# Performance work log

Hardware: AMD Instinct MI355X
Metric: run time of the kernel (lower is better)

## Reference

```python
import jax, jax.numpy as jnp
import numpy as np

BINS = 256
EPS = 1e-8


def _norm255(x):
    # (x - min) / (max - min) * 255, truncated to int (torch .int())
    mx = jnp.max(x, axis=(2, 3), keepdims=True)
    mn = jnp.min(x, axis=(2, 3), keepdims=True)
    return ((x - mn) / (mx - mn) * 255.0).astype(jnp.int32)


def _hist256(x):
    # x int32 [B,C,H,W] -> per-(b,c) 256-bin histogram [B,C,256] float32
    B, C = x.shape[0], x.shape[1]
    flat = x.reshape(B * C, -1)
    rows = jnp.arange(B * C)[:, None]
    h = jnp.zeros((B * C, BINS), jnp.float32).at[rows, flat].add(1.0)
    return h.reshape(B, C, BINS)


def _entropy(x):
    # faithful to Entropy(): p = hist / (H*W); h = -sum p*log(p+1e-8)
    B, C, H, W = x.shape
    p = _hist256(x) / (H * W)
    h = -jnp.sum(p * jnp.log(p + EPS), axis=2)
    return h[:, :, None, None]  # [B,C,1,1]


def _joint_entropy(x_p, x_ms):
    # Faithful to Joint_entropy's quirky count: for each (i,j) it counts pixels
    # where (x_ms==i AND x_p==j) OR (x_ms!=i AND x_p!=j).
    # count[i,j] = 2*J[i,j] + npix - hist_ms[i] - hist_p[j], J = joint histogram.
    B, C, H, W = x_ms.shape
    npix = H * W
    bins = jnp.arange(BINS)
    M = (x_ms.reshape(B, C, npix)[..., None] == bins).astype(jnp.float32)  # [B,C,P,256]
    P = (x_p.reshape(B, npix)[..., None] == bins).astype(jnp.float32)      # [B,P,256]
    J = jnp.einsum('bcpi,bpj->bcij', M, P)                                  # [B,C,256,256]
    hist_ms = jnp.sum(M, axis=2)  # [B,C,256]
    hist_p = jnp.sum(P, axis=1)   # [B,256]
    count = 2.0 * J + npix - hist_ms[:, :, :, None] - hist_p[:, None, None, :]
    p = count / float(BINS * BINS)  # original divides by 256*256, not npix
    h = -jnp.sum(p * jnp.log(p + EPS), axis=(2, 3))
    return h[:, :, None, None]  # [B,C,1,1]


def _channel(f_p, f_ms):
    B, C, H, W = f_p.shape
    f_p_m = jnp.mean(f_p, axis=1, keepdims=True)  # [B,1,H,W]
    # AdaptiveAvgPool2d((16,16)) with H,W divisible by 16 == block mean
    pooled = f_p.reshape(B, C, 16, H // 16, 16, W // 16).mean(axis=(3, 5))
    f_p_a = jnp.mean(pooled, axis=1, keepdims=True)  # [B,1,16,16]
    f_ms_n = _norm255(f_ms)
    f_p_m_n = _norm255(f_p_m)
    f_p_a_n = _norm255(f_p_a)
    h_ms = _entropy(f_ms_n)                 # [B,C,1,1]
    h_p = _entropy(f_p_m_n)                 # [B,1,1,1]
    h_ms_p = _joint_entropy(f_p_a_n, f_ms_n)  # [B,C,1,1]
    mi = h_p + h_ms - h_ms_p
    mi = jax.nn.softmax(mi, axis=1)  # nn.Softmax() on 4D -> dim=1
    return f_ms + f_ms * mi


def _similarity(f_p, f_ms):
    B, C, H, W = f_p.shape
    f_ms_u = jax.image.resize(f_ms, (B, C, H, W), method='bilinear')
    a = f_ms_u.reshape(B, C, -1)
    b = f_p.reshape(B, C, -1)
    a = a - jnp.mean(a, axis=2, keepdims=True)
    b = b - jnp.mean(b, axis=2, keepdims=True)
    na = jnp.sqrt(jnp.sum(a * a, axis=2))  # [B,C] (ms norms)
    nb = jnp.sqrt(jnp.sum(b * b, axis=2))  # [B,C] (p norms)
    s = jnp.einsum('bcp,bdp->bcd', a, b)   # [B,C,C]
    return s / ((na * nb) / 100.0)[:, :, None]


def _spatial(f_p, f_ms):
    B, C, H, W = f_p.shape
    s_m = _similarity(f_p, f_ms)
    mx = jnp.max(s_m, axis=2)        # [B,C]
    idx = jnp.argmax(s_m, axis=2)    # [B,C] best f_p channel per ms channel
    scores = jax.nn.softmax(mx, axis=1)
    brow = jnp.arange(B)[:, None]
    # group score: sum of softmax scores of ms-channels that picked value v
    g = jnp.zeros((B, C), scores.dtype).at[brow, idx].add(scores)
    cnt = jnp.zeros((B, C), jnp.int32).at[brow, idx].add(1)
    k = jnp.min(jnp.sum(cnt > 0, axis=1))  # min #unique over batch
    min_k = (k + 1) // 2                   # ceil(min_k / 2)
    order = jnp.argsort(-g, axis=1)        # descending group score; absent groups (0) sort last
    sorted_scores = jnp.take_along_axis(g, order, axis=1)  # [B,C]
    pos_mask = jnp.arange(C) < min_k       # keep top min_k positions
    z = jnp.where(pos_mask[None, :], sorted_scores, -jnp.inf)
    w = jax.nn.softmax(z, axis=1)          # softmax over selected scores, 0 elsewhere
    gathered = jnp.take_along_axis(f_p, order[:, :, None, None], axis=1)  # [B,C,H,W]
    mask = jnp.sum(w[:, :, None, None] * jax.nn.sigmoid(gathered), axis=1, keepdims=True)
    return f_p + f_p * mask


def setup_inputs() -> dict:
    key = jax.random.key(0)
    k1, k2 = jax.random.split(key)
    f_p = jax.random.normal(k1, (8, 64, 256, 256), dtype=jnp.float32)
    f_ms = jax.random.normal(k2, (8, 64, 16, 16), dtype=jnp.float32)
    return {"f_p": f_p, "f_ms": f_ms}


def reference(f_p, f_ms):
    rel_ms = _channel(f_p, f_ms)
    rel_p = _spatial(f_p, f_ms)
    return (rel_p, rel_ms)
```

## Files before the change

kernel.cpp:

```cpp
#include <hip/hip_runtime.h>

#define BB 8
#define CC 64
#define HP 256
#define WP 256
#define PP 65536
#define QQ 256

__device__ __forceinline__ unsigned encF(float f) {
    unsigned u = __float_as_uint(f);
    return (u & 0x80000000u) ? ~u : (u | 0x80000000u);
}
__device__ __forceinline__ float decF(unsigned u) {
    unsigned b = (u & 0x80000000u) ? (u ^ 0x80000000u) : ~u;
    return __uint_as_float(b);
}

__device__ __forceinline__ double blockSumD(double v, double* red4) {
    int t = threadIdx.x;
    for (int d = 32; d; d >>= 1) v += __shfl_down(v, d, 64);
    __syncthreads();
    if ((t & 63) == 0) red4[t >> 6] = v;
    __syncthreads();
    double r = red4[0] + red4[1] + red4[2] + red4[3];
    __syncthreads();
    return r;
}

__global__ __launch_bounds__(256) void k0_init(unsigned* __restrict__ minmax) {
    int t = threadIdx.x;
    if (t < BB) { minmax[2 * t] = 0xFFFFFFFFu; minmax[2 * t + 1] = 0u; }
}

__global__ __launch_bounds__(256) void k3_chan(const float* __restrict__ fp,
                                               float* __restrict__ cellsum,
                                               float* __restrict__ gtent,
                                               float* __restrict__ chsum,
                                               float* __restrict__ chsumsq) {
    int blk = blockIdx.x, b = blk >> 6, c = blk & 63;
    int x = threadIdx.x, s = x >> 4, r = x & 15;
    const float* src = fp + (size_t)(b * CC + c) * PP;
    __shared__ float tentL[256];
    __shared__ double red4[4];
    tentL[x] = 0.0f;
    __syncthreads();
    float wm, w0, wp;
    if (x <= 7)        { wm = 0.f; w0 = 1.f; wp = 0.f; }
    else if (x >= 248) { wm = 0.f; w0 = 1.f; wp = 0.f; }
    else if (r < 8)    { float fx = ((float)r + 8.5f) * 0.0625f; wm = 1.f - fx; w0 = fx;       wp = 0.f; }
    else               { float fx = ((float)r - 7.5f) * 0.0625f; wm = 0.f;      w0 = 1.f - fx; wp = fx;  }
    double sum = 0.0, ssq = 0.0;
    for (int q = 0; q < 16; ++q) {
        float am = 0.f, a0 = 0.f, ap = 0.f, cs = 0.f;
#pragma unroll
        for (int ry = 0; ry < 16; ++ry) {
            float v = src[(q * 16 + ry) * 256 + x];
            sum += (double)v;
            ssq += (double)v * (double)v;
            cs  += v;
            if ((q == 0 && ry < 8) || (q == 15 && ry >= 8)) {
                a0 += v;
            } else if (ry < 8) {
                float fy = ((float)ry + 8.5f) * 0.0625f;
                am += (1.f - fy) * v; a0 += fy * v;
            } else {
                float fy = ((float)ry - 7.5f) * 0.0625f;
                a0 += (1.f - fy) * v; ap += fy * v;
            }
        }
        float vals[10];
        vals[0] = am * wm; vals[1] = am * w0; vals[2] = am * wp;
        vals[3] = a0 * wm; vals[4] = a0 * w0; vals[5] = a0 * wp;
        vals[6] = ap * wm; vals[7] = ap * w0; vals[8] = ap * wp;
        vals[9] = cs;
#pragma unroll
        for (int d = 8; d; d >>= 1) {
#pragma unroll
            for (int k2 = 0; k2 < 10; ++k2) vals[k2] += __shfl_down(vals[k2], d, 16);
        }
        if (r == 0) {
            if (q > 0) {
                if (s > 0)  atomicAdd(&tentL[(q - 1) * 16 + (s - 1)], vals[0]);
                atomicAdd(&tentL[(q - 1) * 16 + s], vals[1]);
                if (s < 15) atomicAdd(&tentL[(q - 1) * 16 + (s + 1)], vals[2]);
            }
            if (s > 0)  atomicAdd(&tentL[q * 16 + (s - 1)], vals[3]);
            atomicAdd(&tentL[q * 16 + s], vals[4]);
            if (s < 15) atomicAdd(&tentL[q * 16 + (s + 1)], vals[5]);
            if (q < 15) {
                if (s > 0)  atomicAdd(&tentL[(q + 1) * 16 + (s - 1)], vals[6]);
                atomicAdd(&tentL[(q + 1) * 16 + s], vals[7]);
                if (s < 15) atomicAdd(&tentL[(q + 1) * 16 + (s + 1)], vals[8]);
            }
            cellsum[(size_t)(b * CC + c) * QQ + q * 16 + s] = vals[9];
        }
    }
    __syncthreads();
    gtent[(size_t)(b * CC + c) * QQ + x] = tentL[x];
    double st = blockSumD(sum, red4);
    double sq = blockSumD(ssq, red4);
    if (x == 0) { chsum[b * CC + c] = (float)st; chsumsq[b * CC + c] = (float)sq; }
}

__global__ __launch_bounds__(256) void k4_ms(const float* __restrict__ fms,
                                             int* __restrict__ msn,
                                             int* __restrict__ histms,
                                             float* __restrict__ hmsE,
                                             float* __restrict__ naArr,
                                             float* __restrict__ mssum) {
    int blk = blockIdx.x, b = blk >> 6, c = blk & 63, t = threadIdx.x;
    __shared__ float m[256];
    __shared__ int hist[256];
    __shared__ double red4[4];
    __shared__ double U[256];
    __shared__ unsigned umn, umx;
    float v = fms[(size_t)(b * CC + c) * QQ + t];
    m[t] = v;
    hist[t] = 0;
    if (t == 0) { umn = 0xFFFFFFFFu; umx = 0u; }
    float mn = v, mx = v;
    for (int d = 32; d; d >>= 1) {
        mn = fminf(mn, __shfl_down(mn, d, 64));
        mx = fmaxf(mx, __shfl_down(mx, d, 64));
    }
    __syncthreads();
    if ((t & 63) == 0) { atomicMin(&umn, encF(mn)); atomicMax(&umx, encF(mx)); }
    __syncthreads();
    mn = decF(umn); mx = decF(umx);
    int bin = (int)((v - mn) / (mx - mn) * 255.0f);
    bin = min(max(bin, 0), 255);
    msn[(size_t)(b * CC + c) * QQ + t] = bin;
    atomicAdd(&hist[bin], 1);
    __syncthreads();
    histms[(size_t)(b * CC + c) * QQ + t] = hist[t];
    float pf = (float)hist[t] * (1.0f / 256.0f);
    double term = -(double)(pf * __logf(pf + 1e-8f));
    double h = blockSumD(term, red4);
    if (t == 0) hmsE[b * CC + c] = (float)h;
    int i = t >> 4, j = t & 15;
    double kdj = (j == 0 || j == 15) ? 13.328125 : 10.65625;
    double mv = (double)m[t];
    double uu = kdj * mv + 2.671875 * ((j > 0 ? (double)m[t - 1] : 0.0) +
                                       (j < 15 ? (double)m[t + 1] : 0.0));
    U[t] = uu;
    __syncthreads();
    double kdi = (i == 0 || i == 15) ? 13.328125 : 10.65625;
    double vv = kdi * U[t] + 2.671875 * ((i > 0 ? U[t - 16] : 0.0) +
                                         (i < 15 ? U[t + 16] : 0.0));
    double sq = blockSumD(mv * vv, red4);
    double msm = blockSumD(mv, red4);
    if (t == 0) {
        mssum[b * CC + c] = (float)msm;
        double meanu = msm * (1.0 / 256.0);
        double na2 = sq - 65536.0 * meanu * meanu;
        naArr[b * CC + c] = (float)sqrt(na2 > 0.0 ? na2 : 0.0);
    }
}

__global__ __launch_bounds__(256) void k8_smax(const float* __restrict__ fms,
                                               const float* __restrict__ gtent,
                                               const float* __restrict__ mssum,
                                               const float* __restrict__ chsum,
                                               const float* __restrict__ chsumsq,
                                               const float* __restrict__ naArr,
                                               float* __restrict__ mxArr,
                                               int* __restrict__ idxArr) {
    int blk = blockIdx.x, b = blk >> 6, c = blk & 63, t = threadIdx.x;
    __shared__ float msrow[256];
    __shared__ double part[256];
    __shared__ double sval[64];
    msrow[t] = fms[(size_t)(b * CC + c) * QQ + t];
    __syncthreads();
    int d = t >> 2, pr = t & 3;
    const float* g = gtent + (size_t)(b * CC + d) * QQ + pr * 64;
    const float* mr = msrow + pr * 64;
    double acc = 0.0;
    for (int q2 = 0; q2 < 64; ++q2) acc += (double)mr[q2] * (double)g[q2];
    part[t] = acc;
    __syncthreads();
    if (t < 64) {
        double meanu = (double)mssum[b * CC + c] * (1.0 / 256.0);
        double meanp = (double)chsum[b * CC + t] * (1.0 / 65536.0);
        sval[t] = part[t * 4] + part[t * 4 + 1] + part[t * 4 + 2] + part[t * 4 + 3]
                  - 65536.0 * meanu * meanp;
    }
    __syncthreads();
    if (t == 0) {
        double best = sval[0]; int bi2 = 0;
        for (int dd = 1; dd < 64; ++dd) { if (sval[dd] > best) { best = sval[dd]; bi2 = dd; } }
        double nac = (double)naArr[b * CC + c];
        double sc_ = (double)chsum[b * CC + c];
        double sq_ = (double)chsumsq[b * CC + c];
        double nb2 = sq_ - sc_ * sc_ * (1.0 / 65536.0);
        double nbc = sqrt(nb2 > 0.0 ? nb2 : 0.0);
        mxArr[b * CC + c] = (float)(best * 100.0 / (nac * nbc));
        idxArr[b * CC + c] = bi2;
    }
}

__global__ __launch_bounds__(512) void k9_small(const float* __restrict__ mxArr,
                                                const int* __restrict__ idxArr,
                                                float* __restrict__ wsel,
                                                int* __restrict__ chanA,
                                                int* __restrict__ minkA) {
    __shared__ double sc[8][64];
    __shared__ double gs[8][64];
    __shared__ int idxS[8][64];
    __shared__ int ordv[8][64];
    __shared__ int uarr[8];
    __shared__ int mkS;
    int t = threadIdx.x;
    int b = t >> 6, c = t & 63;
    double v = (double)mxArr[b * 64 + c];
    double mx = v;
    for (int d = 32; d; d >>= 1) mx = fmax(mx, __shfl_down(mx, d, 64));
    mx = __shfl(mx, 0, 64);
    double e = exp(v - mx);
    double s = e;
    for (int d = 32; d; d >>= 1) s += __shfl_down(s, d, 64);
    s = __shfl(s, 0, 64);
    sc[b][c] = e / s;
    idxS[b][c] = idxArr[b * 64 + c];
    __syncthreads();
    double g = 0.0; int cnt = 0;
    for (int c2 = 0; c2 < 64; ++c2) {
        if (idxS[b][c2] == c) { g += sc[b][c2]; cnt++; }
    }
    gs[b][c] = g;
    unsigned long long ball = __ballot(cnt > 0);
    if (c == 0) uarr[b] = __popcll(ball);
    __syncthreads();
    if (t == 0) {
        int k = uarr[0];
        for (int b2 = 1; b2 < 8; ++b2) k = min(k, uarr[b2]);
        mkS = (k + 1) >> 1;
        minkA[0] = mkS;
    }
    __syncthreads();
    int rk = 0;
    double myg = gs[b][c];
    for (int c3 = 0; c3 < 64; ++c3) {
        double a = gs[b][c3];
        if (a > myg || (a == myg && c3 < c)) rk++;
    }
    ordv[b][rk] = c;
    __syncthreads();
    int mk = mkS;
    double z0 = gs[b][ordv[b][0]];
    double ee = (c < mk) ? exp(gs[b][ordv[b][c]] - z0) : 0.0;
    double se = ee;
    for (int d = 32; d; d >>= 1) se += __shfl_down(se, d, 64);
    se = __shfl(se, 0, 64);
    if (c < mk) {
        wsel[b * 64 + c] = (float)(ee / se);
        chanA[b * 64 + c] = ordv[b][c];
    }
}

__global__ __launch_bounds__(256) void k10_relp(const float* __restrict__ fp,
                                                const float* __restrict__ wsel,
                                                const int* __restrict__ chanA,
                                                const int* __restrict__ minkA,
                                                float* __restrict__ outp,
                                                float* __restrict__ fpm,
                                                unsigned* __restrict__ minmax) {
    int b = blockIdx.y;
    int i4 = blockIdx.x * 256 + threadIdx.x;
    int mk = minkA[0];
    const float4* src = (const float4*)(fp + (size_t)b * CC * PP);
    float mx0 = 0.f, mx1 = 0.f, mx2 = 0.f, mx3 = 0.f;
    for (int i = 0; i < mk; ++i) {
        int ch = chanA[b * 64 + i];
        float wv = wsel[b * 64 + i];
        float4 v = src[(size_t)ch * (PP / 4) + i4];
        mx0 += wv * (1.0f / (1.0f + __expf(-v.x)));
        mx1 += wv * (1.0f / (1.0f + __expf(-v.y)));
        mx2 += wv * (1.0f / (1.0f + __expf(-v.z)));
        mx3 += wv * (1.0f / (1.0f + __expf(-v.w)));
    }
    float sx = 0.f, sy = 0.f, sz = 0.f, sw = 0.f;
    float4* dst = (float4*)(outp + (size_t)b * CC * PP);
    for (int c2 = 0; c2 < CC; ++c2) {
        float4 v = src[(size_t)c2 * (PP / 4) + i4];
        sx += v.x; sy += v.y; sz += v.z; sw += v.w;
        float4 o;
        o.x = v.x + v.x * mx0;
        o.y = v.y + v.y * mx1;
        o.z = v.z + v.z * mx2;
        o.w = v.w + v.w * mx3;
        dst[(size_t)c2 * (PP / 4) + i4] = o;
    }
    const float inv = 1.0f / 64.0f;
    float4 m; m.x = sx * inv; m.y = sy * inv; m.z = sz * inv; m.w = sw * inv;
    ((float4*)(fpm + (size_t)b * PP))[i4] = m;
    float mn = fminf(fminf(m.x, m.y), fminf(m.z, m.w));
    float mxv = fmaxf(fmaxf(m.x, m.y), fmaxf(m.z, m.w));
    for (int d = 32; d; d >>= 1) {
        mn = fminf(mn, __shfl_down(mn, d, 64));
        mxv = fmaxf(mxv, __shfl_down(mxv, d, 64));
    }
    __shared__ unsigned smn, smx;
    if (threadIdx.x == 0) { smn = 0xFFFFFFFFu; smx = 0u; }
    __syncthreads();
    if ((threadIdx.x & 63) == 0) { atomicMin(&smn, encF(mn)); atomicMax(&smx, encF(mxv)); }
    __syncthreads();
    if (threadIdx.x == 0) { atomicMin(&minmax[2 * b], smn); atomicMax(&minmax[2 * b + 1], smx); }
}

__global__ __launch_bounds__(256) void kC_small(const float* __restrict__ fpm,
                                                const unsigned* __restrict__ minmax,
                                                const float* __restrict__ cellsum,
                                                float* __restrict__ hpE,
                                                int* __restrict__ pan,
                                                int* __restrict__ histp) {
    int b = blockIdx.x, t = threadIdx.x;
    __shared__ int hist[256];
    __shared__ double red4[4];
    __shared__ unsigned umn, umx;
    hist[t] = 0;
    if (t == 0) { umn = 0xFFFFFFFFu; umx = 0u; }
    __syncthreads();
    float mn = decF(minmax[2 * b]);
    float mx = decF(minmax[2 * b + 1]);
    float dd = mx - mn;
    const float4* src = (const float4*)(fpm + (size_t)b * PP);
    for (int i4 = t; i4 < PP / 4; i4 += 256) {
        float4 v = src[i4];
        int b0 = (int)((v.x - mn) / dd * 255.0f);
        int b1 = (int)((v.y - mn) / dd * 255.0f);
        int b2 = (int)((v.z - mn) / dd * 255.0f);
        int b3 = (int)((v.w - mn) / dd * 255.0f);
        b0 = min(max(b0, 0), 255); b1 = min(max(b1, 0), 255);
        b2 = min(max(b2, 0), 255); b3 = min(max(b3, 0), 255);
        atomicAdd(&hist[b0], 1); atomicAdd(&hist[b1], 1);
        atomicAdd(&hist[b2], 1); atomicAdd(&hist[b3], 1);
    }
    __syncthreads();
    int n = hist[t];
    float p = (float)n * (1.0f / 65536.0f);
    double term = -(double)(p * __logf(p + 1e-8f));
    double h = blockSumD(term, red4);
    if (t == 0) hpE[b] = (float)h;
    __syncthreads();
    hist[t] = 0;
    __syncthreads();
    double acc = 0.0;
    for (int c = 0; c < CC; ++c) acc += (double)cellsum[(size_t)(b * CC + c) * QQ + t];
    float pa = (float)(acc * (1.0 / 256.0) * (1.0 / 64.0));
    float mn2 = pa, mx2 = pa;
    for (int d = 32; d; d >>= 1) {
        mn2 = fminf(mn2, __shfl_down(mn2, d, 64));
        mx2 = fmaxf(mx2, __shfl_down(mx2, d, 64));
    }
    __syncthreads();
    if ((t & 63) == 0) { atomicMin(&umn, encF(mn2)); atomicMax(&umx, encF(mx2)); }
    __syncthreads();
    mn2 = decF(umn); mx2 = decF(umx);
    int bin = (int)((pa - mn2) / (mx2 - mn2) * 255.0f);
    bin = min(max(bin, 0), 255);
    pan[b * QQ + t] = bin;
    atomicAdd(&hist[bin], 1);
    __syncthreads();
    histp[b * 256 + t] = hist[t];
}

__global__ __launch_bounds__(256) void k6_joint(const int* __restrict__ msn,
                                                const int* __restrict__ pan,
                                                const int* __restrict__ histms,
                                                const int* __restrict__ histp,
                                                float* __restrict__ hjoint) {
    int blk = blockIdx.x, b = blk >> 6, c = blk & 63, t = threadIdx.x;
    __shared__ int key[256], hms[256], hp[256];
    __shared__ double red4[4];
    int iv = msn[(size_t)(b * CC + c) * QQ + t];
    int jv = pan[b * QQ + t];
    key[t] = (iv << 8) | jv;
    hms[t] = histms[(size_t)(b * CC + c) * QQ + t];
    hp[t] = histp[b * 256 + t];
    __syncthreads();
    unsigned long long w0_ = 0, w1_ = 0, w2_ = 0, w3_ = 0;
    for (int p = 0; p < 256; ++p) {
        int k2 = key[p];
        if ((k2 >> 8) == t) {
            int j = k2 & 255;
            unsigned long long bit = 1ull << (j & 63);
            int w = j >> 6;
            if (w == 0) w0_ |= bit; else if (w == 1) w1_ |= bit;
            else if (w == 2) w2_ |= bit; else w3_ |= bit;
        }
    }
    double acc = 0.0;
    int basei = 256 - hms[t];
    unsigned long long words[4] = { w0_, w1_, w2_, w3_ };
#pragma unroll
    for (int w = 0; w < 4; ++w) {
        unsigned long long word = words[w];
        for (int jj = 0; jj < 64; ++jj) {
            if (!((word >> jj) & 1ull)) {
                int cnt = basei - hp[w * 64 + jj];
                float pf = (float)cnt * (1.0f / 65536.0f);
                acc -= (double)(pf * __logf(pf + 1e-8f));
            }
        }
    }
    int myk = key[t], n = 0; bool first = true;
    for (int p = 0; p < 256; ++p) {
        int k2 = key[p];
        if (k2 == myk) { n++; if (p < t) first = false; }
    }
    if (first) {
        int cnt = 2 * n + 256 - hms[myk >> 8] - hp[myk & 255];
        float pf = (float)cnt * (1.0f / 65536.0f);
        acc -= (double)(pf * __logf(pf + 1e-8f));
    }
    double h = blockSumD(acc, red4);
    if (t == 0) hjoint[b * CC + c] = (float)h;
}

__global__ __launch_bounds__(256) void k7_relms(const float* __restrict__ fms,
                                                const float* __restrict__ hmsE,
                                                const float* __restrict__ hpE,
                                                const float* __restrict__ hjoint,
                                                float* __restrict__ out2) {
    int b = blockIdx.x, t = threadIdx.x;
    __shared__ double mi[64];
    if (t < 64) mi[t] = (double)hpE[b] + (double)hmsE[b * CC + t] - (double)hjoint[b * CC + t];
    __syncthreads();
    if (t == 0) {
        double mxv = mi[0];
        for (int c2 = 1; c2 < 64; ++c2) if (mi[c2] > mxv) mxv = mi[c2];
        double s = 0.0;
        for (int c2 = 0; c2 < 64; ++c2) { mi[c2] = exp(mi[c2] - mxv); s += mi[c2]; }
        for (int c2 = 0; c2 < 64; ++c2) mi[c2] /= s;
    }
    __syncthreads();
    const float* src = fms + (size_t)b * CC * QQ;
    float* dst = out2 + (size_t)b * CC * QQ;
    for (int e = t; e < CC * QQ; e += 256) {
        float v = src[e];
        float miv = (float)mi[e >> 8];
        dst[e] = v + v * miv;
    }
}

extern "C" void kernel_launch(void* const* d_in, const int* in_sizes, int n_in,
                              void* d_out, int out_size, void* d_ws, size_t ws_size,
                              hipStream_t stream) {
    const float* fp = (const float*)d_in[0];
    const float* fms = (const float*)d_in[1];
    float* out = (float*)d_out;

    char* p = (char*)d_ws;
    auto alloc = [&](size_t bytes) { void* r = (void*)p; p += (bytes + 255) & ~(size_t)255; return r; };

    float* fpm      = (float*)alloc((size_t)BB * PP * 4);
    float* cellsum  = (float*)alloc((size_t)BB * CC * QQ * 4);
    float* gtent    = (float*)alloc((size_t)BB * CC * QQ * 4);
    float* chsum    = (float*)alloc((size_t)BB * CC * 4);
    float* chsumsq  = (float*)alloc((size_t)BB * CC * 4);
    unsigned* minmax= (unsigned*)alloc((size_t)BB * 2 * 4);
    int* msn        = (int*)alloc((size_t)BB * CC * QQ * 4);
    int* histms     = (int*)alloc((size_t)BB * CC * 256 * 4);
    int* histp      = (int*)alloc((size_t)BB * 256 * 4);
    int* pan        = (int*)alloc((size_t)BB * QQ * 4);
    float* hmsE     = (float*)alloc((size_t)BB * CC * 4);
    float* hpE      = (float*)alloc((size_t)BB * 4);
    float* hjoint   = (float*)alloc((size_t)BB * CC * 4);
    float* naArr    = (float*)alloc((size_t)BB * CC * 4);
    float* mssum    = (float*)alloc((size_t)BB * CC * 4);
    float* mxArr    = (float*)alloc((size_t)BB * CC * 4);
    int* idxArr     = (int*)alloc((size_t)BB * CC * 4);
    float* wsel     = (float*)alloc((size_t)BB * CC * 4);
    int* chanA      = (int*)alloc((size_t)BB * CC * 4);
    int* minkA      = (int*)alloc(256);

    float* out_relp  = out;
    float* out_relms = out + (size_t)BB * CC * PP;

    k0_init<<<1, 256, 0, stream>>>(minmax);
    k3_chan<<<512, 256, 0, stream>>>(fp, cellsum, gtent, chsum, chsumsq);
    k4_ms<<<512, 256, 0, stream>>>(fms, msn, histms, hmsE, naArr, mssum);
    k8_smax<<<512, 256, 0, stream>>>(fms, gtent, mssum, chsum, chsumsq, naArr, mxArr, idxArr);
    k9_small<<<1, 512, 0, stream>>>(mxArr, idxArr, wsel, chanA, minkA);
    k10_relp<<<dim3(64, 8), 256, 0, stream>>>(fp, wsel, chanA, minkA, out_relp, fpm, minmax);
    kC_small<<<8, 256, 0, stream>>>(fpm, minmax, cellsum, hpE, pan, histp);
    k6_joint<<<512, 256, 0, stream>>>(msn, pan, histms, histp, hjoint);
    k7_relms<<<8, 256, 0, stream>>>(fms, hmsE, hpE, hjoint, out_relms);
}
```

Measured before the change: 420.9 us.

## Split channel, mask, and histogram kernels into more blocks with atomic merges

The channel-statistics kernel is split four ways along rows, going from 512 to 2048 blocks. Partial tent sums and the double-precision channel sums are merged with global atomics into buffers zeroed by a widened init kernel. The mask computation moves out of the output kernel into its own kernel, and the 8-block histogram kernel becomes a 512-block histogram pass followed by a small finish kernel. The aim is to fill more compute units in the under-parallel stages, at the cost of extra launches, atomics and an extra mask buffer round-trip through memory.

```diff
diff --git a/kernel.cpp b/kernel.cpp
--- a/kernel.cpp
+++ b/kernel.cpp
@@ -27,17 +27,25 @@
     return r;
 }
 
-__global__ __launch_bounds__(256) void k0_init(unsigned* __restrict__ minmax) {
-    int t = threadIdx.x;
+__global__ __launch_bounds__(256) void k0_zero(float* __restrict__ gtent,
+                                               double* __restrict__ chsumD,
+                                               double* __restrict__ chsumsqD,
+                                               int* __restrict__ histpm,
+                                               unsigned* __restrict__ minmax) {
+    int t = blockIdx.x * 256 + threadIdx.x;
+    gtent[t] = 0.f;
+    if (t < BB * CC) { chsumD[t] = 0.0; chsumsqD[t] = 0.0; }
+    if (t < BB * 256) histpm[t] = 0;
     if (t < BB) { minmax[2 * t] = 0xFFFFFFFFu; minmax[2 * t + 1] = 0u; }
 }
 
 __global__ __launch_bounds__(256) void k3_chan(const float* __restrict__ fp,
                                                float* __restrict__ cellsum,
                                                float* __restrict__ gtent,
-                                               float* __restrict__ chsum,
-                                               float* __restrict__ chsumsq) {
-    int blk = blockIdx.x, b = blk >> 6, c = blk & 63;
+                                               double* __restrict__ chsumD,
+                                               double* __restrict__ chsumsqD) {
+    int blk = blockIdx.x;
+    int qg = blk & 3, c = (blk >> 2) & 63, b = blk >> 8;
     int x = threadIdx.x, s = x >> 4, r = x & 15;
     const float* src = fp + (size_t)(b * CC + c) * PP;
     __shared__ float tentL[256];
@@ -50,7 +58,8 @@
     else if (r < 8)    { float fx = ((float)r + 8.5f) * 0.0625f; wm = 1.f - fx; w0 = fx;       wp = 0.f; }
     else               { float fx = ((float)r - 7.5f) * 0.0625f; wm = 0.f;      w0 = 1.f - fx; wp = fx;  }
     double sum = 0.0, ssq = 0.0;
-    for (int q = 0; q < 16; ++q) {
+    for (int qi = 0; qi < 4; ++qi) {
+        int q = qg * 4 + qi;
         float am = 0.f, a0 = 0.f, ap = 0.f, cs = 0.f;
 #pragma unroll
         for (int ry = 0; ry < 16; ++ry) {
@@ -96,10 +105,18 @@
         }
     }
     __syncthreads();
-    gtent[(size_t)(b * CC + c) * QQ + x] = tentL[x];
+    int row = x >> 4;
+    int rlo = qg * 4 - 1; if (rlo < 0) rlo = 0;
+    int rhi = qg * 4 + 4; if (rhi > 15) rhi = 15;
+    if (row >= rlo && row <= rhi) {
+        atomicAdd(&gtent[(size_t)(b * CC + c) * QQ + x], tentL[x]);
+    }
     double st = blockSumD(sum, red4);
     double sq = blockSumD(ssq, red4);
-    if (x == 0) { chsum[b * CC + c] = (float)st; chsumsq[b * CC + c] = (float)sq; }
+    if (x == 0) {
+        atomicAdd(&chsumD[b * CC + c], st);
+        atomicAdd(&chsumsqD[b * CC + c], sq);
+    }
 }
 
 __global__ __launch_bounds__(256) void k4_ms(const float* __restrict__ fms,
@@ -160,8 +177,8 @@
 __global__ __launch_bounds__(256) void k8_smax(const float* __restrict__ fms,
                                                const float* __restrict__ gtent,
                                                const float* __restrict__ mssum,
-                                               const float* __restrict__ chsum,
-                                               const float* __restrict__ chsumsq,
+                                               const double* __restrict__ chsumD,
+                                               const double* __restrict__ chsumsqD,
                                                const float* __restrict__ naArr,
                                                float* __restrict__ mxArr,
                                                int* __restrict__ idxArr) {
@@ -180,7 +197,7 @@
     __syncthreads();
     if (t < 64) {
         double meanu = (double)mssum[b * CC + c] * (1.0 / 256.0);
-        double meanp = (double)chsum[b * CC + t] * (1.0 / 65536.0);
+        double meanp = chsumD[b * CC + t] * (1.0 / 65536.0);
         sval[t] = part[t * 4] + part[t * 4 + 1] + part[t * 4 + 2] + part[t * 4 + 3]
                   - 65536.0 * meanu * meanp;
     }
@@ -189,8 +206,8 @@
         double best = sval[0]; int bi2 = 0;
         for (int dd = 1; dd < 64; ++dd) { if (sval[dd] > best) { best = sval[dd]; bi2 = dd; } }
         double nac = (double)naArr[b * CC + c];
-        double sc_ = (double)chsum[b * CC + c];
-        double sq_ = (double)chsumsq[b * CC + c];
+        double sc_ = chsumD[b * CC + c];
+        double sq_ = chsumsqD[b * CC + c];
         double nb2 = sq_ - sc_ * sc_ * (1.0 / 65536.0);
         double nbc = sqrt(nb2 > 0.0 ? nb2 : 0.0);
         mxArr[b * CC + c] = (float)(best * 100.0 / (nac * nbc));
@@ -257,13 +274,11 @@
     }
 }
 
-__global__ __launch_bounds__(256) void k10_relp(const float* __restrict__ fp,
-                                                const float* __restrict__ wsel,
-                                                const int* __restrict__ chanA,
-                                                const int* __restrict__ minkA,
-                                                float* __restrict__ outp,
-                                                float* __restrict__ fpm,
-                                                unsigned* __restrict__ minmax) {
+__global__ __launch_bounds__(256) void kM_mask(const float* __restrict__ fp,
+                                               const float* __restrict__ wsel,
+                                               const int* __restrict__ chanA,
+                                               const int* __restrict__ minkA,
+                                               float* __restrict__ maskB) {
     int b = blockIdx.y;
     int i4 = blockIdx.x * 256 + threadIdx.x;
     int mk = minkA[0];
@@ -278,16 +293,28 @@
         mx2 += wv * (1.0f / (1.0f + __expf(-v.z)));
         mx3 += wv * (1.0f / (1.0f + __expf(-v.w)));
     }
+    ((float4*)(maskB + (size_t)b * PP))[i4] = make_float4(mx0, mx1, mx2, mx3);
+}
+
+__global__ __launch_bounds__(256) void k10_relp(const float* __restrict__ fp,
+                                                const float* __restrict__ maskB,
+                                                float* __restrict__ outp,
+                                                float* __restrict__ fpm,
+                                                unsigned* __restrict__ minmax) {
+    int b = blockIdx.y;
+    int i4 = blockIdx.x * 256 + threadIdx.x;
+    const float4* src = (const float4*)(fp + (size_t)b * CC * PP);
+    float4 mk4 = ((const float4*)(maskB + (size_t)b * PP))[i4];
     float sx = 0.f, sy = 0.f, sz = 0.f, sw = 0.f;
     float4* dst = (float4*)(outp + (size_t)b * CC * PP);
     for (int c2 = 0; c2 < CC; ++c2) {
         float4 v = src[(size_t)c2 * (PP / 4) + i4];
         sx += v.x; sy += v.y; sz += v.z; sw += v.w;
         float4 o;
-        o.x = v.x + v.x * mx0;
-        o.y = v.y + v.y * mx1;
-        o.z = v.z + v.z * mx2;
-        o.w = v.w + v.w * mx3;
+        o.x = v.x + v.x * mk4.x;
+        o.y = v.y + v.y * mk4.y;
+        o.z = v.z + v.z * mk4.z;
+        o.w = v.w + v.w * mk4.w;
         dst[(size_t)c2 * (PP / 4) + i4] = o;
     }
     const float inv = 1.0f / 64.0f;
@@ -307,43 +334,46 @@
     if (threadIdx.x == 0) { atomicMin(&minmax[2 * b], smn); atomicMax(&minmax[2 * b + 1], smx); }
 }
 
-__global__ __launch_bounds__(256) void kC_small(const float* __restrict__ fpm,
+__global__ __launch_bounds__(256) void k2a_hist(const float* __restrict__ fpm,
                                                 const unsigned* __restrict__ minmax,
-                                                const float* __restrict__ cellsum,
-                                                float* __restrict__ hpE,
-                                                int* __restrict__ pan,
-                                                int* __restrict__ histp) {
+                                                int* __restrict__ histpm) {
+    int b = blockIdx.y;
+    __shared__ int h[256];
+    h[threadIdx.x] = 0;
+    __syncthreads();
+    float mn = decF(minmax[2 * b]);
+    float mx = decF(minmax[2 * b + 1]);
+    float dd = mx - mn;
+    int i4 = blockIdx.x * 256 + threadIdx.x;
+    float4 v = ((const float4*)(fpm + (size_t)b * PP))[i4];
+    int b0 = (int)((v.x - mn) / dd * 255.0f);
+    int b1 = (int)((v.y - mn) / dd * 255.0f);
+    int b2 = (int)((v.z - mn) / dd * 255.0f);
+    int b3 = (int)((v.w - mn) / dd * 255.0f);
+    b0 = min(max(b0, 0), 255); b1 = min(max(b1, 0), 255);
+    b2 = min(max(b2, 0), 255); b3 = min(max(b3, 0), 255);
+    atomicAdd(&h[b0], 1); atomicAdd(&h[b1], 1);
+    atomicAdd(&h[b2], 1); atomicAdd(&h[b3], 1);
+    __syncthreads();
+    atomicAdd(&histpm[b * 256 + threadIdx.x], h[threadIdx.x]);
+}
+
+__global__ __launch_bounds__(256) void kCb_small(const int* __restrict__ histpm,
+                                                 const float* __restrict__ cellsum,
+                                                 float* __restrict__ hpE,
+                                                 int* __restrict__ pan,
+                                                 int* __restrict__ histp) {
     int b = blockIdx.x, t = threadIdx.x;
     __shared__ int hist[256];
     __shared__ double red4[4];
     __shared__ unsigned umn, umx;
     hist[t] = 0;
     if (t == 0) { umn = 0xFFFFFFFFu; umx = 0u; }
-    __syncthreads();
-    float mn = decF(minmax[2 * b]);
-    float mx = decF(minmax[2 * b + 1]);
-    float dd = mx - mn;
-    const float4* src = (const float4*)(fpm + (size_t)b * PP);
-    for (int i4 = t; i4 < PP / 4; i4 += 256) {
-        float4 v = src[i4];
-        int b0 = (int)((v.x - mn) / dd * 255.0f);
-        int b1 = (int)((v.y - mn) / dd * 255.0f);
-        int b2 = (int)((v.z - mn) / dd * 255.0f);
-        int b3 = (int)((v.w - mn) / dd * 255.0f);
-        b0 = min(max(b0, 0), 255); b1 = min(max(b1, 0), 255);
-        b2 = min(max(b2, 0), 255); b3 = min(max(b3, 0), 255);
-        atomicAdd(&hist[b0], 1); atomicAdd(&hist[b1], 1);
-        atomicAdd(&hist[b2], 1); atomicAdd(&hist[b3], 1);
-    }
-    __syncthreads();
-    int n = hist[t];
+    int n = histpm[b * 256 + t];
     float p = (float)n * (1.0f / 65536.0f);
     double term = -(double)(p * __logf(p + 1e-8f));
     double h = blockSumD(term, red4);
     if (t == 0) hpE[b] = (float)h;
-    __syncthreads();
-    hist[t] = 0;
-    __syncthreads();
     double acc = 0.0;
     for (int c = 0; c < CC; ++c) acc += (double)cellsum[(size_t)(b * CC + c) * QQ + t];
     float pa = (float)(acc * (1.0 / 256.0) * (1.0 / 64.0));
@@ -454,11 +484,13 @@
     auto alloc = [&](size_t bytes) { void* r = (void*)p; p += (bytes + 255) & ~(size_t)255; return r; };
 
     float* fpm      = (float*)alloc((size_t)BB * PP * 4);
+    float* maskB    = (float*)alloc((size_t)BB * PP * 4);
     float* cellsum  = (float*)alloc((size_t)BB * CC * QQ * 4);
     float* gtent    = (float*)alloc((size_t)BB * CC * QQ * 4);
-    float* chsum    = (float*)alloc((size_t)BB * CC * 4);
-    float* chsumsq  = (float*)alloc((size_t)BB * CC * 4);
+    double* chsumD  = (double*)alloc((size_t)BB * CC * 8);
+    double* chsumsqD= (double*)alloc((size_t)BB * CC * 8);
     unsigned* minmax= (unsigned*)alloc((size_t)BB * 2 * 4);
+    int* histpm     = (int*)alloc((size_t)BB * 256 * 4);
     int* msn        = (int*)alloc((size_t)BB * CC * QQ * 4);
     int* histms     = (int*)alloc((size_t)BB * CC * 256 * 4);
     int* histp      = (int*)alloc((size_t)BB * 256 * 4);
@@ -477,13 +509,15 @@
     float* out_relp  = out;
     float* out_relms = out + (size_t)BB * CC * PP;
 
-    k0_init<<<1, 256, 0, stream>>>(minmax);
-    k3_chan<<<512, 256, 0, stream>>>(fp, cellsum, gtent, chsum, chsumsq);
+    k0_zero<<<512, 256, 0, stream>>>(gtent, chsumD, chsumsqD, histpm, minmax);
+    k3_chan<<<2048, 256, 0, stream>>>(fp, cellsum, gtent, chsumD, chsumsqD);
     k4_ms<<<512, 256, 0, stream>>>(fms, msn, histms, hmsE, naArr, mssum);
-    k8_smax<<<512, 256, 0, stream>>>(fms, gtent, mssum, chsum, chsumsq, naArr, mxArr, idxArr);
+    k8_smax<<<512, 256, 0, stream>>>(fms, gtent, mssum, chsumD, chsumsqD, naArr, mxArr, idxArr);
     k9_small<<<1, 512, 0, stream>>>(mxArr, idxArr, wsel, chanA, minkA);
-    k10_relp<<<dim3(64, 8), 256, 0, stream>>>(fp, wsel, chanA, minkA, out_relp, fpm, minmax);
-    kC_small<<<8, 256, 0, stream>>>(fpm, minmax, cellsum, hpE, pan, histp);
+    kM_mask<<<dim3(64, 8), 256, 0, stream>>>(fp, wsel, chanA, minkA, maskB);
+    k10_relp<<<dim3(64, 8), 256, 0, stream>>>(fp, maskB, out_relp, fpm, minmax);
+    k2a_hist<<<dim3(64, 8), 256, 0, stream>>>(fpm, minmax, histpm);
+    kCb_small<<<8, 256, 0, stream>>>(histpm, cellsum, hpE, pan, histp);
     k6_joint<<<512, 256, 0, stream>>>(msn, pan, histms, histp, hjoint);
     k7_relms<<<8, 256, 0, stream>>>(fms, hmsE, hpE, hjoint, out_relms);
 }
```

Measured after the change: 413.8 us. About the same (-1.7%).
